# Kernel optimization log

Hardware: AMD Instinct MI355X
Metric: run time of the kernel (lower is better)

## Reference

```python
import jax, jax.numpy as jnp
import numpy as np


def setup_inputs() -> dict:
    key = jax.random.key(0)
    k1, k2 = jax.random.split(key)
    B, S, H, K = 128, 128, 128, 8
    inputs = jax.random.normal(k1, (B, S, H), dtype=jnp.float32)
    threshes = jax.random.uniform(k2, (K,), dtype=jnp.float32)
    return {"inputs": inputs, "threshes": threshes}


def reference(inputs, threshes):
    # Faithful translation of the torch triple loop:
    # a single (B,) accumulator is carried sequentially over
    # (time i, hidden j, neuron k) in row-major order; x[:, i, j] is
    # re-added at every neuron step (first-ever assignment == add to 0).
    B, S, H = inputs.shape
    K = threshes.shape[0]
    x_flat = inputs.reshape(B, S * H).T  # (T, B) with T = S*H

    def outer(s, x_t):  # one (i, j) step
        def inner(s, th):  # one neuron step k
            s = s + x_t
            spike = s > th
            out = jnp.where(spike, s, jnp.zeros((), s.dtype))  # spike * acc
            s = s - out  # reset where spiked
            return s, (out, spike)
        s, (outs, spikes) = jax.lax.scan(inner, s, threshes)  # (K, B)
        return s, (outs, spikes)

    s0 = jnp.zeros((B,), inputs.dtype)
    _, (outs, spikes) = jax.lax.scan(outer, s0, x_flat)  # (T, K, B)

    # (T, K, B) -> (B, S, K, H): torch stacks neurons at dim=1, hidden at dim=2,
    # time at dim=1 of the final stack -> final layout (batch, seq, K, hidden).
    outs = outs.transpose(2, 0, 1).reshape(B, S, H, K).transpose(0, 1, 3, 2)
    spikes = spikes.transpose(2, 0, 1).reshape(B, S, H, K).transpose(0, 1, 3, 2)
    return outs, spikes
```

## Files before the change

### kernel.cpp

```cpp
#include <hip/hip_runtime.h>
#include <math.h>


#define NB 128
#define NS 128
#define NH 128
#define NK 8
#define NT (NS * NH)
#define WL 8
#define NW2 (NT / WL)
#define NG64 (NT / 64)
#define NP64 (NW2 / 64)
#define OUTN ((size_t)NB * NS * NK * NH)

#define WS_M     0
#define WS_SENT  (NB * NW2)
#define WS_TOTAL (2 * NB * NW2)

__global__ void lif_bounds8(const float* __restrict__ x,
                            const float* __restrict__ th,
                            float* __restrict__ M)
{
    int idx = blockIdx.x * 256 + threadIdx.x;
    if (idx >= NB * NW2) return;
    float minth = th[0];
#pragma unroll
    for (int k = 1; k < NK; ++k) minth = fminf(minth, th[k]);
    const float* xp = x + (size_t)idx * WL;
    double p = 0.0, maxp = -1e300;
#pragma unroll
    for (int l = 0; l < WL; ++l) {
        double xv = (double)xp[l];
#pragma unroll
        for (int k = 0; k < NK; ++k) { p += xv; maxp = fmax(maxp, p); }
    }
    M[idx] = (float)((double)minth - maxp - 0.1 - 1e-6 * fabs(maxp));
}

#define ADD8(xv) do { s += xv; s += xv; s += xv; s += xv; \
                      s += xv; s += xv; s += xv; s += xv; } while (0)
#define STEP8(xv) do { \
    s += xv; s = (s > th0) ? 0.0f : s; \
    s += xv; s = (s > th1) ? 0.0f : s; \
    s += xv; s = (s > th2) ? 0.0f : s; \
    s += xv; s = (s > th3) ? 0.0f : s; \
    s += xv; s = (s > th4) ? 0.0f : s; \
    s += xv; s = (s > th5) ? 0.0f : s; \
    s += xv; s = (s > th6) ? 0.0f : s; \
    s += xv; s = (s > th7) ? 0.0f : s; } while (0)

__device__ __forceinline__ float rl(float v, int idx) {
    return __int_as_float(__builtin_amdgcn_readlane(__float_as_int(v), idx));
}

__global__ void __launch_bounds__(64, 1)
lif_chain(const float* __restrict__ x, const float* __restrict__ th,
          const float* __restrict__ M, float* __restrict__ s_ent)
{
    const int b = blockIdx.x;
    const int lane = threadIdx.x;
    const float* xb = x + (size_t)b * NT;
    const float* Mb = M + (size_t)b * NW2;
    float* seb = s_ent + (size_t)b * NW2;

    const float th0 = th[0], th1 = th[1], th2 = th[2], th3 = th[3];
    const float th4 = th[4], th5 = th[5], th6 = th[6], th7 = th[7];

    float s = 0.0f, keep = 0.0f;
    float cx = xb[lane];
    float cM = Mb[lane];

    for (int p = 0; p < NP64; ++p) {
        float nM = Mb[(size_t)((p + 1 < NP64) ? p + 1 : p) * 64 + lane];
        for (int g8 = 0; g8 < 8; ++g8) {
            const int gg = p * 8 + g8;
            float nx = xb[(size_t)((gg + 1 < NG64) ? gg + 1 : gg) * 64 + lane];
#pragma unroll
            for (int wi = 0; wi < 8; ++wi) {
                const int wpi = g8 * 8 + wi;
                float Mc = rl(cM, wpi);
                float x0 = rl(cx, wi * 8 + 0), x1 = rl(cx, wi * 8 + 1);
                float x2 = rl(cx, wi * 8 + 2), x3 = rl(cx, wi * 8 + 3);
                float x4 = rl(cx, wi * 8 + 4), x5 = rl(cx, wi * 8 + 5);
                float x6 = rl(cx, wi * 8 + 6), x7 = rl(cx, wi * 8 + 7);
                keep = (lane == wpi) ? s : keep;
                int q = __builtin_amdgcn_readfirstlane((int)(s <= Mc));
                if (q) {
                    ADD8(x0); ADD8(x1); ADD8(x2); ADD8(x3);
                    ADD8(x4); ADD8(x5); ADD8(x6); ADD8(x7);
                } else {
                    STEP8(x0); STEP8(x1); STEP8(x2); STEP8(x3);
                    STEP8(x4); STEP8(x5); STEP8(x6); STEP8(x7);
                }
            }
            cx = nx;
        }
        seb[(size_t)p * 64 + lane] = keep;
        cM = nM;
    }
}

__global__ void __launch_bounds__(128)
lif_out(const float* __restrict__ x, const float* __restrict__ th,
        const float* __restrict__ s_ent, float* __restrict__ out)
{
    const int j = threadIdx.x;
    const int i = blockIdx.x & (NS - 1);
    const int b = blockIdx.x >> 7;
    const int wl = j >> 3;
    const int r  = j & 7;

    const float th0 = th[0], th1 = th[1], th2 = th[2], th3 = th[3];
    const float th4 = th[4], th5 = th[5], th6 = th[6], th7 = th[7];

    float s = s_ent[(size_t)b * NW2 + i * 16 + wl];
    const float* xrow = x + (size_t)b * NT + i * NH + (wl << 3);

    for (int m = 0; m < r; ++m) {
        float xv = xrow[m];
        STEP8(xv);
    }
    float xv = xrow[r];

    float* o  = out + (((size_t)b * NS + i) * NK) * NH + j;
    float* sp = o + OUTN;
    float thr[NK];
#pragma unroll
    for (int k = 0; k < NK; ++k) thr[k] = th[k];
#pragma unroll
    for (int k = 0; k < NK; ++k) {
        s += xv;
        bool spike = s > thr[k];
        o[(size_t)k * NH]  = spike ? s : 0.0f;
        sp[(size_t)k * NH] = spike ? 1.0f : 0.0f;
        s = spike ? 0.0f : s;
    }
}

__global__ void lif_mono(const float* __restrict__ x, const float* __restrict__ th,
                         float* __restrict__ out)
{
    int b = blockIdx.x * 64 + threadIdx.x;
    if (b >= NB) return;
    float thr[NK];
#pragma unroll
    for (int k = 0; k < NK; ++k) thr[k] = th[k];
    const float* xb = x + (size_t)b * NT;
    float s = 0.0f;
    for (int i = 0; i < NS; ++i)
        for (int j = 0; j < NH; ++j) {
            float xv = xb[i * NH + j];
#pragma unroll
            for (int k = 0; k < NK; ++k) {
                s += xv;
                bool spike = s > thr[k];
                size_t idx = (((size_t)b * NS + i) * NK + k) * NH + j;
                out[idx]        = spike ? s : 0.0f;
                out[OUTN + idx] = spike ? 1.0f : 0.0f;
                s = spike ? 0.0f : s;
            }
        }
}

extern "C" void kernel_launch(void* const* d_in, const int* in_sizes, int n_in,
                              void* d_out, int out_size, void* d_ws, size_t ws_size,
                              hipStream_t stream) {
    const float* x  = (const float*)d_in[0];
    const float* th = (const float*)d_in[1];
    float* out = (float*)d_out;

    if (ws_size >= (size_t)WS_TOTAL * sizeof(float)) {
        float* ws    = (float*)d_ws;
        float* Mbuf  = ws + WS_M;
        float* s_ent = ws + WS_SENT;

        lif_bounds8<<<dim3((NB * NW2 + 255) / 256), dim3(256), 0, stream>>>(x, th, Mbuf);
        lif_chain<<<dim3(NB), dim3(64), 0, stream>>>(x, th, Mbuf, s_ent);
        lif_out<<<dim3(NB * NS), dim3(128), 0, stream>>>(x, th, s_ent, out);
    } else {
        lif_mono<<<dim3(2), dim3(64), 0, stream>>>(x, th, out);
    }
}
```

Before: 464.2 us.

## Add per-64-step no-spike bound and per-threshold tighter window bounds in LIF chain

```diff
diff --git a/kernel.cpp b/kernel.cpp
--- a/kernel.cpp
+++ b/kernel.cpp
@@ -14,27 +14,42 @@
 #define OUTN ((size_t)NB * NS * NK * NH)
 
 #define WS_M     0
-#define WS_SENT  (NB * NW2)
-#define WS_TOTAL (2 * NB * NW2)
-
-__global__ void lif_bounds8(const float* __restrict__ x,
-                            const float* __restrict__ th,
-                            float* __restrict__ M)
+#define WS_M64   (NB * NW2)
+#define WS_SENT  (NB * NW2 + NB * NG64)
+#define WS_TOTAL (2 * NB * NW2 + NB * NG64)
+
+__global__ void lif_bounds(const float* __restrict__ x,
+                           const float* __restrict__ th,
+                           float* __restrict__ M, float* __restrict__ M64)
 {
     int idx = blockIdx.x * 256 + threadIdx.x;
-    if (idx >= NB * NW2) return;
-    float minth = th[0];
-#pragma unroll
-    for (int k = 1; k < NK; ++k) minth = fminf(minth, th[k]);
-    const float* xp = x + (size_t)idx * WL;
-    double p = 0.0, maxp = -1e300;
-#pragma unroll
-    for (int l = 0; l < WL; ++l) {
-        double xv = (double)xp[l];
-#pragma unroll
-        for (int k = 0; k < NK; ++k) { p += xv; maxp = fmax(maxp, p); }
-    }
-    M[idx] = (float)((double)minth - maxp - 0.1 - 1e-6 * fabs(maxp));
+    if (idx >= NB * NG64) return;
+    int b = idx >> 8, gg = idx & (NG64 - 1);
+    float t[NK];
+#pragma unroll
+    for (int k = 0; k < NK; ++k) t[k] = th[k];
+    const float* xp = x + (size_t)b * NT + gg * 64;
+
+    double pg = 0.0, gmax = -1e300;
+#pragma unroll
+    for (int w8 = 0; w8 < 8; ++w8) {
+        double pw = 0.0, wmax = -1e300;
+#pragma unroll
+        for (int l = 0; l < 8; ++l) {
+            double xv = (double)xp[w8 * 8 + l];
+#pragma unroll
+            for (int k = 0; k < NK; ++k) {
+                pw += xv;
+                double rel = pw - (double)t[k];
+                wmax = fmax(wmax, rel);
+            }
+        }
+        gmax = fmax(gmax, pg + wmax);
+        pg += pw;
+        M[(size_t)b * NW2 + gg * 8 + w8] =
+            (float)(-wmax - 0.1 - 1e-6 * fabs(wmax));
+    }
+    M64[(size_t)b * NG64 + gg] = (float)(-gmax - 0.5 - 1e-6 * fabs(gmax));
 }
 
 #define ADD8(xv) do { s += xv; s += xv; s += xv; s += xv; \
@@ -55,45 +70,74 @@
 
 __global__ void __launch_bounds__(64, 1)
 lif_chain(const float* __restrict__ x, const float* __restrict__ th,
-          const float* __restrict__ M, float* __restrict__ s_ent)
+          const float* __restrict__ M, const float* __restrict__ M64,
+          float* __restrict__ s_ent)
 {
     const int b = blockIdx.x;
     const int lane = threadIdx.x;
-    const float* xb = x + (size_t)b * NT;
-    const float* Mb = M + (size_t)b * NW2;
+    const float* xb   = x + (size_t)b * NT;
+    const float* Mb   = M + (size_t)b * NW2;
+    const float* M64b = M64 + (size_t)b * NG64;
     float* seb = s_ent + (size_t)b * NW2;
 
     const float th0 = th[0], th1 = th[1], th2 = th[2], th3 = th[3];
     const float th4 = th[4], th5 = th[5], th6 = th[6], th7 = th[7];
 
     float s = 0.0f, keep = 0.0f;
-    float cx = xb[lane];
-    float cM = Mb[lane];
+    float cx   = xb[lane];
+    float cM   = Mb[lane];
+    float cM64 = M64b[0];
 
     for (int p = 0; p < NP64; ++p) {
         float nM = Mb[(size_t)((p + 1 < NP64) ? p + 1 : p) * 64 + lane];
         for (int g8 = 0; g8 < 8; ++g8) {
             const int gg = p * 8 + g8;
-            float nx = xb[(size_t)((gg + 1 < NG64) ? gg + 1 : gg) * 64 + lane];
-#pragma unroll
-            for (int wi = 0; wi < 8; ++wi) {
-                const int wpi = g8 * 8 + wi;
-                float Mc = rl(cM, wpi);
-                float x0 = rl(cx, wi * 8 + 0), x1 = rl(cx, wi * 8 + 1);
-                float x2 = rl(cx, wi * 8 + 2), x3 = rl(cx, wi * 8 + 3);
-                float x4 = rl(cx, wi * 8 + 4), x5 = rl(cx, wi * 8 + 5);
-                float x6 = rl(cx, wi * 8 + 6), x7 = rl(cx, wi * 8 + 7);
-                keep = (lane == wpi) ? s : keep;
-                int q = __builtin_amdgcn_readfirstlane((int)(s <= Mc));
-                if (q) {
-                    ADD8(x0); ADD8(x1); ADD8(x2); ADD8(x3);
-                    ADD8(x4); ADD8(x5); ADD8(x6); ADD8(x7);
-                } else {
-                    STEP8(x0); STEP8(x1); STEP8(x2); STEP8(x3);
-                    STEP8(x4); STEP8(x5); STEP8(x6); STEP8(x7);
+            const int ggn = (gg + 1 < NG64) ? gg + 1 : gg;
+            float nx   = xb[(size_t)ggn * 64 + lane];
+            float nM64 = M64b[ggn];
+            const int wbase = g8 * 8;
+
+            int q64 = __builtin_amdgcn_readfirstlane((int)(s <= cM64));
+            if (q64) {
+                float xc = rl(cx, 0);
+#pragma unroll
+                for (int wi = 0; wi < 8; ++wi) {
+                    keep = (lane == wbase + wi) ? s : keep;
+#pragma unroll
+                    for (int m = 0; m < 8; ++m) {
+                        int ni = wi * 8 + m + 1; if (ni > 63) ni = 63;
+                        float xn = rl(cx, ni);
+                        ADD8(xc);
+                        xc = xn;
+                    }
+                }
+            } else {
+#pragma unroll
+                for (int wi = 0; wi < 8; ++wi) {
+                    float Mc = rl(cM, wbase + wi);
+                    keep = (lane == wbase + wi) ? s : keep;
+                    float xc = rl(cx, wi * 8);
+                    int q = __builtin_amdgcn_readfirstlane((int)(s <= Mc));
+                    if (q) {
+#pragma unroll
+                        for (int m = 0; m < 8; ++m) {
+                            int ni = wi * 8 + m + 1; if (ni > 63) ni = 63;
+                            float xn = rl(cx, ni);
+                            ADD8(xc);
+                            xc = xn;
+                        }
+                    } else {
+#pragma unroll
+                        for (int m = 0; m < 8; ++m) {
+                            int ni = wi * 8 + m + 1; if (ni > 63) ni = 63;
+                            float xn = rl(cx, ni);
+                            STEP8(xc);
+                            xc = xn;
+                        }
+                    }
                 }
             }
-            cx = nx;
+            cx = nx; cM64 = nM64;
         }
         seb[(size_t)p * 64 + lane] = keep;
         cM = nM;
@@ -172,10 +216,11 @@
     if (ws_size >= (size_t)WS_TOTAL * sizeof(float)) {
         float* ws    = (float*)d_ws;
         float* Mbuf  = ws + WS_M;
+        float* M64b  = ws + WS_M64;
         float* s_ent = ws + WS_SENT;
 
-        lif_bounds8<<<dim3((NB * NW2 + 255) / 256), dim3(256), 0, stream>>>(x, th, Mbuf);
-        lif_chain<<<dim3(NB), dim3(64), 0, stream>>>(x, th, Mbuf, s_ent);
+        lif_bounds<<<dim3((NB * NG64 + 255) / 256), dim3(256), 0, stream>>>(x, th, Mbuf, M64b);
+        lif_chain<<<dim3(NB), dim3(64), 0, stream>>>(x, th, Mbuf, M64b, s_ent);
         lif_out<<<dim3(NB * NS), dim3(128), 0, stream>>>(x, th, s_ent, out);
     } else {
         lif_mono<<<dim3(2), dim3(64), 0, stream>>>(x, th, out);
```

Result: faster. 417.2 us (-10.1%).

## Skip 64-step groups in LIF chain via precomputed record-reset states

Applied to the files above, without the earlier changes.

```diff
diff --git a/kernel.cpp b/kernel.cpp
--- a/kernel.cpp
+++ b/kernel.cpp
@@ -7,34 +7,20 @@
 #define NH 128
 #define NK 8
 #define NT (NS * NH)
-#define WL 8
-#define NW2 (NT / WL)
+#define NW2 (NT / 8)
 #define NG64 (NT / 64)
-#define NP64 (NW2 / 64)
 #define OUTN ((size_t)NB * NS * NK * NH)
 
-#define WS_M     0
-#define WS_SENT  (NB * NW2)
-#define WS_TOTAL (2 * NB * NW2)
-
-__global__ void lif_bounds8(const float* __restrict__ x,
-                            const float* __restrict__ th,
-                            float* __restrict__ M)
-{
-    int idx = blockIdx.x * 256 + threadIdx.x;
-    if (idx >= NB * NW2) return;
-    float minth = th[0];
-#pragma unroll
-    for (int k = 1; k < NK; ++k) minth = fminf(minth, th[k]);
-    const float* xp = x + (size_t)idx * WL;
-    double p = 0.0, maxp = -1e300;
-#pragma unroll
-    for (int l = 0; l < WL; ++l) {
-        double xv = (double)xp[l];
-#pragma unroll
-        for (int k = 0; k < NK; ++k) { p += xv; maxp = fmax(maxp, p); }
-    }
-    M[idx] = (float)((double)minth - maxp - 0.1 - 1e-6 * fabs(maxp));
+#define WS_SENT2 0
+#define WS_SENT  (NB * NG64)
+#define WS_HI    (WS_SENT + NB * NW2)
+#define WS_LO    (WS_HI + NB * NG64 * 16)
+#define WS_PK    (WS_LO + NB * NG64 * 16)
+#define WS_JT    (WS_PK + NB * NG64 * 16)
+#define WS_TOT   (WS_JT + NB * NG64 * 16)
+
+__device__ __forceinline__ float rl(float v, int idx) {
+    return __int_as_float(__builtin_amdgcn_readlane(__float_as_int(v), idx));
 }
 
 #define ADD8(xv) do { s += xv; s += xv; s += xv; s += xv; \
@@ -49,55 +35,202 @@
     s += xv; s = (s > th6) ? 0.0f : s; \
     s += xv; s = (s > th7) ? 0.0f : s; } while (0)
 
-__device__ __forceinline__ float rl(float v, int idx) {
-    return __int_as_float(__builtin_amdgcn_readlane(__float_as_int(v), idx));
-}
+#define RSLOT(i) \
+    v##i = (rec && nr == i) ? m : v##i; \
+    j##i = (rec && nr == i) ? ss : j##i;
+
+__global__ void __launch_bounds__(256)
+lif_rec(const float* __restrict__ x, const float* __restrict__ th,
+        float* __restrict__ HI, float* __restrict__ LO, int* __restrict__ JT)
+{
+    int idx = blockIdx.x * 256 + threadIdx.x;
+    if (idx >= NB * NG64) return;
+    int b = idx >> 8, gg = idx & (NG64 - 1);
+    const float* xg = x + (size_t)b * NT + gg * 64;
+    const float t0 = th[0], t1 = th[1], t2 = th[2], t3 = th[3];
+    const float t4 = th[4], t5 = th[5], t6 = th[6], t7 = th[7];
+
+    double p = 0.0, rmin = 1e300, map = 0.0;
+    double v0 = 0, v1 = 0, v2 = 0, v3 = 0, v4 = 0, v5 = 0, v6 = 0, v7 = 0;
+    double v8 = 0, v9 = 0, v10 = 0, v11 = 0, v12 = 0, v13 = 0, v14 = 0;
+    int j0 = 512, j1 = 512, j2 = 512, j3 = 512, j4 = 512, j5 = 512, j6 = 512;
+    int j7 = 512, j8 = 512, j9 = 512, j10 = 512, j11 = 512, j12 = 512;
+    int j13 = 512, j14 = 512;
+    int nr = 0;
+
+    for (int ti = 0; ti < 64; ++ti) {
+        double xv = (double)xg[ti];
+#pragma unroll
+        for (int k = 0; k < 8; ++k) {
+            p += xv;
+            map = fmax(map, fabs(p));
+            double tk = (k == 0) ? t0 : (k == 1) ? t1 : (k == 2) ? t2 :
+                        (k == 3) ? t3 : (k == 4) ? t4 : (k == 5) ? t5 :
+                        (k == 6) ? t6 : t7;
+            double m = tk - p;
+            bool rec = m < rmin;
+            rmin = rec ? m : rmin;
+            const int ss = ti * 8 + k;
+            RSLOT(0) RSLOT(1) RSLOT(2) RSLOT(3) RSLOT(4)
+            RSLOT(5) RSLOT(6) RSLOT(7) RSLOT(8) RSLOT(9)
+            RSLOT(10) RSLOT(11) RSLOT(12) RSLOT(13) RSLOT(14)
+            nr = rec ? nr + 1 : nr;
+        }
+    }
+
+    const double mg  = 3.2e-5 * (2.0 * map + 2.0) + 1e-3;
+    const double m15 = 3.2e-5 * (map + 65536.0) + 1e-3;
+    size_t base = (size_t)idx * 16;
+#define STSLOT(i) { bool val = (j##i < 512); \
+    HI[base + i] = val ? (float)(v##i + mg) : 3.0e38f; \
+    LO[base + i] = val ? (float)(v##i - mg) : 3.0e38f; \
+    JT[base + i] = j##i; }
+    STSLOT(0) STSLOT(1) STSLOT(2) STSLOT(3) STSLOT(4)
+    STSLOT(5) STSLOT(6) STSLOT(7) STSLOT(8) STSLOT(9)
+    STSLOT(10) STSLOT(11) STSLOT(12) STSLOT(13) STSLOT(14)
+#undef STSLOT
+    HI[base + 15] = 3.0e38f;
+    LO[base + 15] = (float)(rmin - m15);
+    JT[base + 15] = 512;
+}
+
+__global__ void __launch_bounds__(256)
+lif_cont(const float* __restrict__ x, const float* __restrict__ th,
+         const int* __restrict__ JT, float* __restrict__ PK)
+{
+    int idx = blockIdx.x * 256 + threadIdx.x;
+    if (idx >= NB * NG64 * 16) return;
+    int b = idx >> 12;
+    int r = idx & 4095;
+    int gg = r >> 4;
+    int j = JT[idx];
+    float out = 0.0f;
+    if (j < 512) {
+        const float* xg = x + (size_t)b * NT + gg * 64;
+        const float th0 = th[0], th1 = th[1], th2 = th[2], th3 = th[3];
+        const float th4 = th[4], th5 = th[5], th6 = th[6], th7 = th[7];
+        int jt = j >> 3, jk = j & 7;
+        float s = 0.0f;
+        {
+            float xv = xg[jt];
+#pragma unroll
+            for (int k = 0; k < 8; ++k) {
+                float tk = (k == 0) ? th0 : (k == 1) ? th1 : (k == 2) ? th2 :
+                           (k == 3) ? th3 : (k == 4) ? th4 : (k == 5) ? th5 :
+                           (k == 6) ? th6 : th7;
+                float ns = s + xv;
+                ns = (ns > tk) ? 0.0f : ns;
+                s = (k > jk) ? ns : s;
+            }
+        }
+        for (int ti = jt + 1; ti < 64; ++ti) {
+            float xv = xg[ti];
+            STEP8(xv);
+        }
+        out = s;
+    }
+    PK[idx] = out;
+}
+
+#define PROCESS(cH, cL, cK, cx, ggexpr) do { \
+    const int _gg = (ggexpr); \
+    keep = (lane == (_gg & 63)) ? s : keep; \
+    unsigned long long _bH = __ballot(s > (cH)); \
+    unsigned long long _bL = __ballot(s > (cL)); \
+    unsigned _hi = (unsigned)_bH & 0xffffu; \
+    unsigned _lo = (unsigned)_bL & 0xffffu; \
+    int _ii = __ffs((int)_hi); \
+    unsigned _below = _ii ? (_lo & ((1u << (_ii - 1)) - 1u)) : _lo; \
+    int _cls = (_ii && _below == 0u) ? 1 : ((_lo == 0u) ? 2 : 0); \
+    _cls = __builtin_amdgcn_readfirstlane(_cls); \
+    if (_cls == 1) { \
+        s = rl((cK), _ii - 1);             \
+    } else if (_cls == 2) { \
+        for (int _w = 0; _w < 8; ++_w) {   \
+            _Pragma("unroll") \
+            for (int _m = 0; _m < 8; ++_m) { \
+                float _xc = rl((cx), _w * 8 + _m); \
+                ADD8(_xc); \
+            } \
+        } \
+    } else { \
+        for (int _w = 0; _w < 8; ++_w) {   \
+            _Pragma("unroll") \
+            for (int _m = 0; _m < 8; ++_m) { \
+                float _xc = rl((cx), _w * 8 + _m); \
+                STEP8(_xc); \
+            } \
+        } \
+    } \
+} while (0)
 
 __global__ void __launch_bounds__(64, 1)
-lif_chain(const float* __restrict__ x, const float* __restrict__ th,
-          const float* __restrict__ M, float* __restrict__ s_ent)
+lif_chain_g(const float* __restrict__ x, const float* __restrict__ th,
+            const float* __restrict__ HI, const float* __restrict__ LO,
+            const float* __restrict__ PK, float* __restrict__ seb2)
 {
     const int b = blockIdx.x;
     const int lane = threadIdx.x;
-    const float* xb = x + (size_t)b * NT;
-    const float* Mb = M + (size_t)b * NW2;
-    float* seb = s_ent + (size_t)b * NW2;
+    const int l16 = lane & 15;
+    const float* xb  = x  + (size_t)b * NT;
+    const float* HIb = HI + (size_t)b * NG64 * 16;
+    const float* LOb = LO + (size_t)b * NG64 * 16;
+    const float* PKb = PK + (size_t)b * NG64 * 16;
+    float* se2 = seb2 + (size_t)b * NG64;
 
     const float th0 = th[0], th1 = th[1], th2 = th[2], th3 = th[3];
     const float th4 = th[4], th5 = th[5], th6 = th[6], th7 = th[7];
 
     float s = 0.0f, keep = 0.0f;
-    float cx = xb[lane];
-    float cM = Mb[lane];
-
-    for (int p = 0; p < NP64; ++p) {
-        float nM = Mb[(size_t)((p + 1 < NP64) ? p + 1 : p) * 64 + lane];
-        for (int g8 = 0; g8 < 8; ++g8) {
-            const int gg = p * 8 + g8;
-            float nx = xb[(size_t)((gg + 1 < NG64) ? gg + 1 : gg) * 64 + lane];
-#pragma unroll
-            for (int wi = 0; wi < 8; ++wi) {
-                const int wpi = g8 * 8 + wi;
-                float Mc = rl(cM, wpi);
-                float x0 = rl(cx, wi * 8 + 0), x1 = rl(cx, wi * 8 + 1);
-                float x2 = rl(cx, wi * 8 + 2), x3 = rl(cx, wi * 8 + 3);
-                float x4 = rl(cx, wi * 8 + 4), x5 = rl(cx, wi * 8 + 5);
-                float x6 = rl(cx, wi * 8 + 6), x7 = rl(cx, wi * 8 + 7);
-                keep = (lane == wpi) ? s : keep;
-                int q = __builtin_amdgcn_readfirstlane((int)(s <= Mc));
-                if (q) {
-                    ADD8(x0); ADD8(x1); ADD8(x2); ADD8(x3);
-                    ADD8(x4); ADD8(x5); ADD8(x6); ADD8(x7);
-                } else {
-                    STEP8(x0); STEP8(x1); STEP8(x2); STEP8(x3);
-                    STEP8(x4); STEP8(x5); STEP8(x6); STEP8(x7);
-                }
-            }
-            cx = nx;
-        }
-        seb[(size_t)p * 64 + lane] = keep;
-        cM = nM;
-    }
+    float cHa = HIb[l16],      cLa = LOb[l16],      cKa = PKb[l16];
+    float cHb = HIb[16 + l16], cLb = LOb[16 + l16], cKb = PKb[16 + l16];
+    float cxa = xb[lane], cxb = xb[64 + lane];
+
+    for (int sg = 0; sg < 4; ++sg) {
+        for (int gp = 0; gp < 32; ++gp) {
+            const int gg = sg * 64 + gp * 2;
+            int gn = gg + 2; if (gn > NG64 - 2) gn = NG64 - 2;
+            float nHa = HIb[(size_t)gn * 16 + l16];
+            float nLa = LOb[(size_t)gn * 16 + l16];
+            float nKa = PKb[(size_t)gn * 16 + l16];
+            float nHb = HIb[(size_t)(gn + 1) * 16 + l16];
+            float nLb = LOb[(size_t)(gn + 1) * 16 + l16];
+            float nKb = PKb[(size_t)(gn + 1) * 16 + l16];
+            float nxa = xb[(size_t)gn * 64 + lane];
+            float nxb = xb[(size_t)(gn + 1) * 64 + lane];
+
+            PROCESS(cHa, cLa, cKa, cxa, gg);
+            PROCESS(cHb, cLb, cKb, cxb, gg + 1);
+
+            cHa = nHa; cLa = nLa; cKa = nKa; cxa = nxa;
+            cHb = nHb; cLb = nLb; cKb = nKb; cxb = nxb;
+        }
+        se2[sg * 64 + lane] = keep;
+    }
+}
+
+__global__ void __launch_bounds__(256)
+lif_replay(const float* __restrict__ x, const float* __restrict__ th,
+           const float* __restrict__ seb2, float* __restrict__ s_ent)
+{
+    int idx = blockIdx.x * 256 + threadIdx.x;
+    if (idx >= NB * NG64 * 8) return;
+    int b = idx >> 11;
+    int r = idx & 2047;
+    int gg = r >> 3;
+    int w = r & 7;
+
+    const float th0 = th[0], th1 = th[1], th2 = th[2], th3 = th[3];
+    const float th4 = th[4], th5 = th[5], th6 = th[6], th7 = th[7];
+
+    float s = seb2[(size_t)b * NG64 + gg];
+    const float* xg = x + (size_t)b * NT + gg * 64;
+    const int nt = w * 8;
+    for (int ti = 0; ti < nt; ++ti) {
+        float xv = xg[ti];
+        STEP8(xv);
+    }
+    s_ent[(size_t)b * NW2 + gg * 8 + w] = s;
 }
 
 __global__ void __launch_bounds__(128)
@@ -168,14 +301,20 @@
     const float* x  = (const float*)d_in[0];
     const float* th = (const float*)d_in[1];
     float* out = (float*)d_out;
-
-    if (ws_size >= (size_t)WS_TOTAL * sizeof(float)) {
-        float* ws    = (float*)d_ws;
-        float* Mbuf  = ws + WS_M;
+    float* ws  = (float*)d_ws;
+
+    if (ws_size >= (size_t)WS_TOT * sizeof(float)) {
+        float* seb2  = ws + WS_SENT2;
         float* s_ent = ws + WS_SENT;
-
-        lif_bounds8<<<dim3((NB * NW2 + 255) / 256), dim3(256), 0, stream>>>(x, th, Mbuf);
-        lif_chain<<<dim3(NB), dim3(64), 0, stream>>>(x, th, Mbuf, s_ent);
+        float* HIb   = ws + WS_HI;
+        float* LOb   = ws + WS_LO;
+        float* PKb   = ws + WS_PK;
+        int*   JTb   = (int*)(ws + WS_JT);
+
+        lif_rec<<<dim3((NB * NG64 + 255) / 256), dim3(256), 0, stream>>>(x, th, HIb, LOb, JTb);
+        lif_cont<<<dim3((NB * NG64 * 16 + 255) / 256), dim3(256), 0, stream>>>(x, th, JTb, PKb);
+        lif_chain_g<<<dim3(NB), dim3(64), 0, stream>>>(x, th, HIb, LOb, PKb, seb2);
+        lif_replay<<<dim3((NB * NG64 * 8 + 255) / 256), dim3(256), 0, stream>>>(x, th, seb2, s_ent);
         lif_out<<<dim3(NB * NS), dim3(128), 0, stream>>>(x, th, s_ent, out);
     } else {
         lif_mono<<<dim3(2), dim3(64), 0, stream>>>(x, th, out);
```

Measured after the change: 666.4 us. +43.6%, slower.
